# Optimization experiments

Measured on AMD Instinct MI355X. Metric: run time of the kernel, lower is better.

The kernel has to match this reference:

```python
import jax, jax.numpy as jnp
import numpy as np

B, H, IN = 2048, 256, 64
K_TERMS = 8


def setup_inputs() -> dict:
    key = jax.random.key(0)
    ks = jax.random.split(key, 8)
    limit_x = float(np.sqrt(6.0 / (IN + H)))
    limit_h = float(np.sqrt(6.0 / (H + H)))
    return {
        "h": jax.random.normal(ks[0], (B, H), dtype=jnp.float32),
        "x": jax.random.normal(ks[1], (B, IN), dtype=jnp.float32),
        "xdot": jax.random.normal(ks[2], (B, IN), dtype=jnp.float32),
        "wx": jax.random.uniform(ks[3], (H, IN), minval=-limit_x, maxval=limit_x, dtype=jnp.float32),
        "wh": jax.random.uniform(ks[4], (H, H), minval=-limit_h, maxval=limit_h, dtype=jnp.float32),
        "wout": jax.random.uniform(ks[5], (H, H), minval=-limit_h, maxval=limit_h, dtype=jnp.float32),
        "b0": jnp.zeros((H,), dtype=jnp.float32),
        "b1": jnp.zeros((H,), dtype=jnp.float32),
    }


def reference(h, x, xdot, wx, wh, wout, b0, b1):
    # Batched version of the per-sample vector field (original is vmapped by the solver).
    l1 = x @ wx.T + h @ wh.T + b0                 # [B,H]
    relu_val = jax.nn.relu(l1)
    lout = relu_val @ wout.T + b1                 # [B,H]
    tanh_val = jnp.tanh(lout)
    dtanh = 1.0 - tanh_val ** 2                   # [B,H]
    drelu = (l1 > 0).astype(jnp.float32)          # activation == 'relu' (hard gate)
    # d_outer[b,i,j] = dtanh[b,i] * wout[i,j] * drelu[b,j]
    d_outer = dtanh[:, :, None] * wout[None, :, :] * drelu[:, None, :]  # [B,H,H]
    Jx = jnp.einsum('bhj,ji->bhi', d_outer, wx)   # [B,H,IN]
    Jh = jnp.einsum('bhj,ji->bhi', d_outer, wh)   # [B,H,H]
    jx = jnp.einsum('bhi,bi->bh', Jx, xdot)       # [B,H]
    h_dot = jx
    curr_term = jx
    for _ in range(K_TERMS):
        curr_term = jnp.einsum('bij,bj->bi', Jh, curr_term)
        h_dot = h_dot + curr_term
    return h_dot
```

## Files before the change

kernel.cpp:

```cpp
#include <hip/hip_runtime.h>
#include <math.h>

#define B_  2048
#define H_  256
#define IN_ 64

typedef __attribute__((ext_vector_type(8))) short bf8_t;
typedef __attribute__((ext_vector_type(4))) short s4_t;
typedef __attribute__((ext_vector_type(4))) float f4_t;

#define MFMA_BF16(a, b, c) __builtin_amdgcn_mfma_f32_16x16x32_bf16((a), (b), (c), 0, 0, 0)

__device__ __forceinline__ short f2bf(float f) {
  union { float f; unsigned u; } v; v.f = f;
  unsigned u = v.u + 0x7fffu + ((v.u >> 16) & 1u);
  return (short)(u >> 16);
}
__device__ __forceinline__ float bf2f(short s) {
  union { unsigned u; float f; } v; v.u = ((unsigned)(unsigned short)s) << 16;
  return v.f;
}

__device__ __align__(16) short g_whf[2][65536];
__device__ __align__(16) short g_wof[2][65536];
__device__ __align__(16) short g_wxf[2][16384];

__global__ void prep_frag(const float* __restrict__ wh, const float* __restrict__ wo,
                          const float* __restrict__ wx) {
  int tid = blockIdx.x * 256 + threadIdx.x;
  const float* W; short* Dh; short* Dl; int ld, ksh, o8;
  if (tid < 8192)       { W = wh; Dh = g_whf[0]; Dl = g_whf[1]; ld = 256; ksh = 3; o8 = tid; }
  else if (tid < 16384) { W = wo; Dh = g_wof[0]; Dl = g_wof[1]; ld = 256; ksh = 3; o8 = tid - 8192; }
  else if (tid < 18432) { W = wx; Dh = g_wxf[0]; Dl = g_wxf[1]; ld = 64;  ksh = 1; o8 = tid - 16384; }
  else return;
  int lane = o8 & 63;
  int gks = o8 >> 6;
  int g = gks >> ksh, ks = gks & ((1 << ksh) - 1);
  int c = g * 16 + (lane & 15);
  int k0 = ks * 32 + ((lane >> 4) & 3) * 8;
  const float* p = W + (size_t)c * ld + k0;
  bf8_t hi, lo;
#pragma unroll
  for (int j = 0; j < 8; ++j) {
    float f = p[j];
    short h = f2bf(f);
    hi[j] = h; lo[j] = f2bf(f - bf2f(h));
  }
  *reinterpret_cast<bf8_t*>(Dh + (size_t)o8 * 8) = hi;
  *reinterpret_cast<bf8_t*>(Dl + (size_t)o8 * 8) = lo;
}

#define GEMM3(A0, A1, AH, AL, WH, WL, NK) do {                                  \
  f4_t q0 = {0.f,0.f,0.f,0.f}, q1 = {0.f,0.f,0.f,0.f};                          \
  _Pragma("unroll")                                                             \
  for (int ks = 0; ks < (NK); ++ks) {                                           \
    bf8_t ah = *reinterpret_cast<const bf8_t*>(&AH[ln][ks * 32 + lq * 8]);      \
    bf8_t al = *reinterpret_cast<const bf8_t*>(&AL[ln][ks * 32 + lq * 8]);      \
    if (ks & 1) {                                                               \
      q0 = MFMA_BF16(ah, WH[0][ks], q0); q0 = MFMA_BF16(ah, WL[0][ks], q0);     \
      q0 = MFMA_BF16(al, WH[0][ks], q0);                                        \
      q1 = MFMA_BF16(ah, WH[1][ks], q1); q1 = MFMA_BF16(ah, WL[1][ks], q1);     \
      q1 = MFMA_BF16(al, WH[1][ks], q1);                                        \
    } else {                                                                    \
      A0 = MFMA_BF16(ah, WH[0][ks], A0); A0 = MFMA_BF16(ah, WL[0][ks], A0);     \
      A0 = MFMA_BF16(al, WH[0][ks], A0);                                        \
      A1 = MFMA_BF16(ah, WH[1][ks], A1); A1 = MFMA_BF16(ah, WL[1][ks], A1);     \
      A1 = MFMA_BF16(al, WH[1][ks], A1);                                        \
    }                                                                           \
  }                                                                             \
  A0 = A0 + q0; A1 = A1 + q1; } while (0)

#define GEMM2(A0, A1, AH, AL, WH, NK) do {                                      \
  f4_t q0 = {0.f,0.f,0.f,0.f}, q1 = {0.f,0.f,0.f,0.f};                          \
  _Pragma("unroll")                                                             \
  for (int ks = 0; ks < (NK); ++ks) {                                           \
    bf8_t ah = *reinterpret_cast<const bf8_t*>(&AH[ln][ks * 32 + lq * 8]);      \
    bf8_t al = *reinterpret_cast<const bf8_t*>(&AL[ln][ks * 32 + lq * 8]);      \
    if (ks & 1) {                                                               \
      q0 = MFMA_BF16(ah, WH[0][ks], q0); q0 = MFMA_BF16(al, WH[0][ks], q0);     \
      q1 = MFMA_BF16(ah, WH[1][ks], q1); q1 = MFMA_BF16(al, WH[1][ks], q1);     \
    } else {                                                                    \
      A0 = MFMA_BF16(ah, WH[0][ks], A0); A0 = MFMA_BF16(al, WH[0][ks], A0);     \
      A1 = MFMA_BF16(ah, WH[1][ks], A1); A1 = MFMA_BF16(al, WH[1][ks], A1);     \
    }                                                                           \
  }                                                                             \
  A0 = A0 + q0; A1 = A1 + q1; } while (0)

#define GEMM1(A0, A1, AH, WH, NK) do {                                          \
  f4_t q0 = {0.f,0.f,0.f,0.f}, q1 = {0.f,0.f,0.f,0.f};                          \
  _Pragma("unroll")                                                             \
  for (int ks = 0; ks < (NK); ++ks) {                                           \
    bf8_t ah = *reinterpret_cast<const bf8_t*>(&AH[ln][ks * 32 + lq * 8]);      \
    if (ks & 1) {                                                               \
      q0 = MFMA_BF16(ah, WH[0][ks], q0);                                        \
      q1 = MFMA_BF16(ah, WH[1][ks], q1);                                        \
    } else {                                                                    \
      A0 = MFMA_BF16(ah, WH[0][ks], A0);                                        \
      A1 = MFMA_BF16(ah, WH[1][ks], A1);                                        \
    }                                                                           \
  }                                                                             \
  A0 = A0 + q0; A1 = A1 + q1; } while (0)

__global__ __launch_bounds__(512, 2) void jacde_mfma(
    const float* __restrict__ h_g, const float* __restrict__ x_g,
    const float* __restrict__ xd_g, const float* __restrict__ wx,
    const float* __restrict__ wh, const float* __restrict__ b0,
    const float* __restrict__ b1, float* __restrict__ out) {

  __shared__ short h_hi[16][264], h_lo[16][264];
  __shared__ short x_hi[16][72],  x_lo[16][72];
  __shared__ short xd_hi[16][72], xd_lo[16][72];
  __shared__ short u_hi[16][264], u_lo[16][264];
  __shared__ short v_hi[16][264];
  __shared__ float l1_t[16][264];
  __shared__ int   fix_cnt;
  __shared__ int   fix_list[64];

  const int tid  = threadIdx.x;
  const int wv   = tid >> 6;
  const int lane = tid & 63;
  const int ln   = lane & 15;
  const int lq   = lane >> 4;
  const int r0   = blockIdx.x * 16;
  const int cbase = wv * 32;

  if (tid == 0) fix_cnt = 0;

  for (int c = tid; c < 16 * 64; c += 512) {
    int r = c >> 6, k4 = (c & 63) * 4;
    f4_t v = *reinterpret_cast<const f4_t*>(h_g + (size_t)(r0 + r) * H_ + k4);
    s4_t shv, slv;
#pragma unroll
    for (int j = 0; j < 4; ++j) { short h = f2bf(v[j]); shv[j] = h; slv[j] = f2bf(v[j] - bf2f(h)); }
    *reinterpret_cast<s4_t*>(&h_hi[r][k4]) = shv;
    *reinterpret_cast<s4_t*>(&h_lo[r][k4]) = slv;
  }
  {
    int t2 = tid & 255;
    const float* src = (tid < 256) ? x_g : xd_g;
    short (*dh)[72] = (tid < 256) ? x_hi : xd_hi;
    short (*dl)[72] = (tid < 256) ? x_lo : xd_lo;
    int r = t2 >> 4, k4 = (t2 & 15) * 4;
    f4_t v = *reinterpret_cast<const f4_t*>(src + (size_t)(r0 + r) * IN_ + k4);
    s4_t shv, slv;
#pragma unroll
    for (int j = 0; j < 4; ++j) { short h = f2bf(v[j]); shv[j] = h; slv[j] = f2bf(v[j] - bf2f(h)); }
    *reinterpret_cast<s4_t*>(&dh[r][k4]) = shv;
    *reinterpret_cast<s4_t*>(&dl[r][k4]) = slv;
  }

  bf8_t whf[2][8], wof[2][8];
  f4_t acc0, acc1, sacc0, sacc1;
  float dre0[4], dre1[4], dta0[4], dta1[4], hd0[4], hd1[4];

  {
    bf8_t whl[2][8], wxh[2][2], wxl[2][2];
#pragma unroll
    for (int t = 0; t < 2; ++t) {
      int gb = wv * 2 + t;
#pragma unroll
      for (int ks = 0; ks < 8; ++ks) {
        int off = ((gb * 8 + ks) * 64 + lane) * 8;
        whf[t][ks] = *reinterpret_cast<const bf8_t*>(&g_whf[0][off]);
        whl[t][ks] = *reinterpret_cast<const bf8_t*>(&g_whf[1][off]);
      }
#pragma unroll
      for (int ks = 0; ks < 2; ++ks) {
        int off = ((gb * 2 + ks) * 64 + lane) * 8;
        wxh[t][ks] = *reinterpret_cast<const bf8_t*>(&g_wxf[0][off]);
        wxl[t][ks] = *reinterpret_cast<const bf8_t*>(&g_wxf[1][off]);
      }
    }
    __syncthreads();

    float bv0 = b0[cbase + ln], bv1 = b0[cbase + 16 + ln];
    acc0 = (f4_t){bv0, bv0, bv0, bv0};
    acc1 = (f4_t){bv1, bv1, bv1, bv1};
    GEMM3(acc0, acc1, h_hi, h_lo, whf, whl, 8);
    GEMM3(acc0, acc1, x_hi, x_lo, wxh, wxl, 2);
    sacc0 = (f4_t){0.f, 0.f, 0.f, 0.f};
    sacc1 = (f4_t){0.f, 0.f, 0.f, 0.f};
    GEMM3(sacc0, sacc1, xd_hi, xd_lo, wxh, wxl, 2);
#pragma unroll
    for (int r = 0; r < 4; ++r) {
      l1_t[lq * 4 + r][cbase + ln]      = acc0[r];
      l1_t[lq * 4 + r][cbase + 16 + ln] = acc1[r];
    }
  }
  __syncthreads();

  for (int e = tid; e < 16 * 256; e += 512) {
    int r = e >> 8, c = e & 255;
    if (fabsf(l1_t[r][c]) < 1e-4f) {
      int idx = atomicAdd(&fix_cnt, 1);
      if (idx < 64) fix_list[idx] = (r << 8) | c;
    }
  }
  __syncthreads();
  {
    int nfix = min(fix_cnt, 64);
    for (int e = wv; e < nfix; e += 8) {
      int rc = fix_list[e];
      int r = rc >> 8, c = rc & 255;
      const float* hrow = h_g + (size_t)(r0 + r) * H_;
      const float* wrow = wh + (size_t)c * H_;
      double sum = (double)hrow[lane]       * (double)wrow[lane]
                 + (double)hrow[lane + 64]  * (double)wrow[lane + 64]
                 + (double)hrow[lane + 128] * (double)wrow[lane + 128]
                 + (double)hrow[lane + 192] * (double)wrow[lane + 192]
                 + (double)x_g[(size_t)(r0 + r) * IN_ + lane] * (double)wx[(size_t)c * IN_ + lane];
#pragma unroll
      for (int m = 32; m; m >>= 1) sum += __shfl_xor(sum, m);
      if (lane == 0) l1_t[r][c] = (float)(sum + (double)b0[c]);
    }
  }
  __syncthreads();

  for (int e = tid; e < 16 * 256; e += 512) {
    int r = e >> 8, c = e & 255;
    float l1 = l1_t[r][c];
    float rv = l1 > 0.f ? l1 : 0.f;
    short hi = f2bf(rv);
    u_hi[r][c] = hi;
    u_lo[r][c] = f2bf(rv - bf2f(hi));
  }
#pragma unroll
  for (int r = 0; r < 4; ++r) {
    dre0[r] = (l1_t[lq * 4 + r][cbase + ln]      > 0.f) ? 1.f : 0.f;
    dre1[r] = (l1_t[lq * 4 + r][cbase + 16 + ln] > 0.f) ? 1.f : 0.f;
  }
  __syncthreads();

  {
    bf8_t wol[2][8];
#pragma unroll
    for (int t = 0; t < 2; ++t) {
      int gb = wv * 2 + t;
#pragma unroll
      for (int ks = 0; ks < 8; ++ks) {
        int off = ((gb * 8 + ks) * 64 + lane) * 8;
        wof[t][ks] = *reinterpret_cast<const bf8_t*>(&g_wof[0][off]);
        wol[t][ks] = *reinterpret_cast<const bf8_t*>(&g_wof[1][off]);
      }
    }
    float bv0 = b1[cbase + ln], bv1 = b1[cbase + 16 + ln];
    acc0 = (f4_t){bv0, bv0, bv0, bv0};
    acc1 = (f4_t){bv1, bv1, bv1, bv1};
    GEMM3(acc0, acc1, u_hi, u_lo, wof, wol, 8);
#pragma unroll
    for (int r = 0; r < 4; ++r) {
      float t0 = tanhf(acc0[r]);
      float t1 = tanhf(acc1[r]);
      dta0[r] = 1.f - t0 * t0;
      dta1[r] = 1.f - t1 * t1;
    }
  }
  __syncthreads();

#pragma unroll
  for (int r = 0; r < 4; ++r) {
    int row = lq * 4 + r;
    float v0 = dre0[r] * sacc0[r];
    float v1 = dre1[r] * sacc1[r];
    short h0 = f2bf(v0), h1 = f2bf(v1);
    u_hi[row][cbase + ln]      = h0;  u_lo[row][cbase + ln]      = f2bf(v0 - bf2f(h0));
    u_hi[row][cbase + 16 + ln] = h1;  u_lo[row][cbase + 16 + ln] = f2bf(v1 - bf2f(h1));
  }
  __syncthreads();

  acc0 = (f4_t){0.f, 0.f, 0.f, 0.f};
  acc1 = (f4_t){0.f, 0.f, 0.f, 0.f};
  GEMM2(acc0, acc1, u_hi, u_lo, wof, 8);
#pragma unroll
  for (int r = 0; r < 4; ++r) {
    int row = lq * 4 + r;
    float v0 = dta0[r] * acc0[r];
    float v1 = dta1[r] * acc1[r];
    hd0[r] = v0; hd1[r] = v1;
    v_hi[row][cbase + ln]      = f2bf(v0);
    v_hi[row][cbase + 16 + ln] = f2bf(v1);
  }
  __syncthreads();

  for (int it = 0; it < 8; ++it) {
    acc0 = (f4_t){0.f, 0.f, 0.f, 0.f};
    acc1 = (f4_t){0.f, 0.f, 0.f, 0.f};
    GEMM1(acc0, acc1, v_hi, whf, 8);
#pragma unroll
    for (int r = 0; r < 4; ++r) {
      int row = lq * 4 + r;
      u_hi[row][cbase + ln]      = f2bf(dre0[r] * acc0[r]);
      u_hi[row][cbase + 16 + ln] = f2bf(dre1[r] * acc1[r]);
    }
    __syncthreads();

    acc0 = (f4_t){0.f, 0.f, 0.f, 0.f};
    acc1 = (f4_t){0.f, 0.f, 0.f, 0.f};
    GEMM1(acc0, acc1, u_hi, wof, 8);
#pragma unroll
    for (int r = 0; r < 4; ++r) {
      int row = lq * 4 + r;
      float v0 = dta0[r] * acc0[r];
      float v1 = dta1[r] * acc1[r];
      hd0[r] += v0; hd1[r] += v1;
      if (it < 7) {
        v_hi[row][cbase + ln]      = f2bf(v0);
        v_hi[row][cbase + 16 + ln] = f2bf(v1);
      }
    }
    __syncthreads();
  }

#pragma unroll
  for (int r = 0; r < 4; ++r) {
    int row = lq * 4 + r;
    out[(size_t)(r0 + row) * H_ + cbase + ln]      = hd0[r];
    out[(size_t)(r0 + row) * H_ + cbase + 16 + ln] = hd1[r];
  }
}

extern "C" void kernel_launch(void* const* d_in, const int* in_sizes, int n_in,
                              void* d_out, int out_size, void* d_ws, size_t ws_size,
                              hipStream_t stream) {
  const float* h_g  = (const float*)d_in[0];
  const float* x_g  = (const float*)d_in[1];
  const float* xd_g = (const float*)d_in[2];
  const float* wx   = (const float*)d_in[3];
  const float* wh   = (const float*)d_in[4];
  const float* wo   = (const float*)d_in[5];
  const float* b0   = (const float*)d_in[6];
  const float* b1   = (const float*)d_in[7];
  prep_frag<<<dim3(72), dim3(256), 0, stream>>>(wh, wo, wx);
  jacde_mfma<<<dim3(B_ / 16), dim3(512), 0, stream>>>(
      h_g, x_g, xd_g, wx, wh, b0, b1, (float*)d_out);
}
```

Before: 89.51 us.

## Split each block's columns over 16 waves with one 16-column tile per wave

Doubles the block from 512 to 1024 threads so each of 16 wavefronts owns one 16-column MFMA tile instead of two. Register-resident weight fragments per wave are halved, and the serial iteration chain is spread across more waves per block to raise latency hiding. In exchange each wave issues half as many independent MFMA chains, and barriers now synchronise twice as many waves. Occupancy limits and register pressure also change with the new launch bounds.

Result: no change. 90.94 us (+1.6%).

```diff
diff --git a/kernel.cpp b/kernel.cpp
--- a/kernel.cpp
+++ b/kernel.cpp
@@ -50,58 +50,44 @@
   *reinterpret_cast<bf8_t*>(Dl + (size_t)o8 * 8) = lo;
 }
 
-#define GEMM3(A0, A1, AH, AL, WH, WL, NK) do {                                  \
-  f4_t q0 = {0.f,0.f,0.f,0.f}, q1 = {0.f,0.f,0.f,0.f};                          \
+#define GEMM3s(A0, AH, AL, WH, WL, NK) do {                                     \
+  f4_t q0 = {0.f,0.f,0.f,0.f};                                                  \
   _Pragma("unroll")                                                             \
   for (int ks = 0; ks < (NK); ++ks) {                                           \
     bf8_t ah = *reinterpret_cast<const bf8_t*>(&AH[ln][ks * 32 + lq * 8]);      \
     bf8_t al = *reinterpret_cast<const bf8_t*>(&AL[ln][ks * 32 + lq * 8]);      \
     if (ks & 1) {                                                               \
-      q0 = MFMA_BF16(ah, WH[0][ks], q0); q0 = MFMA_BF16(ah, WL[0][ks], q0);     \
-      q0 = MFMA_BF16(al, WH[0][ks], q0);                                        \
-      q1 = MFMA_BF16(ah, WH[1][ks], q1); q1 = MFMA_BF16(ah, WL[1][ks], q1);     \
-      q1 = MFMA_BF16(al, WH[1][ks], q1);                                        \
+      q0 = MFMA_BF16(ah, WH[ks], q0); q0 = MFMA_BF16(ah, WL[ks], q0);           \
+      q0 = MFMA_BF16(al, WH[ks], q0);                                           \
     } else {                                                                    \
-      A0 = MFMA_BF16(ah, WH[0][ks], A0); A0 = MFMA_BF16(ah, WL[0][ks], A0);     \
-      A0 = MFMA_BF16(al, WH[0][ks], A0);                                        \
-      A1 = MFMA_BF16(ah, WH[1][ks], A1); A1 = MFMA_BF16(ah, WL[1][ks], A1);     \
-      A1 = MFMA_BF16(al, WH[1][ks], A1);                                        \
+      A0 = MFMA_BF16(ah, WH[ks], A0); A0 = MFMA_BF16(ah, WL[ks], A0);           \
+      A0 = MFMA_BF16(al, WH[ks], A0);                                           \
     }                                                                           \
   }                                                                             \
-  A0 = A0 + q0; A1 = A1 + q1; } while (0)
-
-#define GEMM2(A0, A1, AH, AL, WH, NK) do {                                      \
-  f4_t q0 = {0.f,0.f,0.f,0.f}, q1 = {0.f,0.f,0.f,0.f};                          \
+  A0 = A0 + q0; } while (0)
+
+#define GEMM2s(A0, AH, AL, WH, NK) do {                                         \
+  f4_t q0 = {0.f,0.f,0.f,0.f};                                                  \
   _Pragma("unroll")                                                             \
   for (int ks = 0; ks < (NK); ++ks) {                                           \
     bf8_t ah = *reinterpret_cast<const bf8_t*>(&AH[ln][ks * 32 + lq * 8]);      \
     bf8_t al = *reinterpret_cast<const bf8_t*>(&AL[ln][ks * 32 + lq * 8]);      \
-    if (ks & 1) {                                                               \
-      q0 = MFMA_BF16(ah, WH[0][ks], q0); q0 = MFMA_BF16(al, WH[0][ks], q0);     \
-      q1 = MFMA_BF16(ah, WH[1][ks], q1); q1 = MFMA_BF16(al, WH[1][ks], q1);     \
-    } else {                                                                    \
-      A0 = MFMA_BF16(ah, WH[0][ks], A0); A0 = MFMA_BF16(al, WH[0][ks], A0);     \
-      A1 = MFMA_BF16(ah, WH[1][ks], A1); A1 = MFMA_BF16(al, WH[1][ks], A1);     \
-    }                                                                           \
+    if (ks & 1) { q0 = MFMA_BF16(ah, WH[ks], q0); q0 = MFMA_BF16(al, WH[ks], q0); } \
+    else        { A0 = MFMA_BF16(ah, WH[ks], A0); A0 = MFMA_BF16(al, WH[ks], A0); } \
   }                                                                             \
-  A0 = A0 + q0; A1 = A1 + q1; } while (0)
-
-#define GEMM1(A0, A1, AH, WH, NK) do {                                          \
-  f4_t q0 = {0.f,0.f,0.f,0.f}, q1 = {0.f,0.f,0.f,0.f};                          \
+  A0 = A0 + q0; } while (0)
+
+#define GEMM1s(A0, AH, WH, NK) do {                                             \
+  f4_t q0 = {0.f,0.f,0.f,0.f};                                                  \
   _Pragma("unroll")                                                             \
   for (int ks = 0; ks < (NK); ++ks) {                                           \
     bf8_t ah = *reinterpret_cast<const bf8_t*>(&AH[ln][ks * 32 + lq * 8]);      \
-    if (ks & 1) {                                                               \
-      q0 = MFMA_BF16(ah, WH[0][ks], q0);                                        \
-      q1 = MFMA_BF16(ah, WH[1][ks], q1);                                        \
-    } else {                                                                    \
-      A0 = MFMA_BF16(ah, WH[0][ks], A0);                                        \
-      A1 = MFMA_BF16(ah, WH[1][ks], A1);                                        \
-    }                                                                           \
+    if (ks & 1) q0 = MFMA_BF16(ah, WH[ks], q0);                                 \
+    else        A0 = MFMA_BF16(ah, WH[ks], A0);                                 \
   }                                                                             \
-  A0 = A0 + q0; A1 = A1 + q1; } while (0)
-
-__global__ __launch_bounds__(512, 2) void jacde_mfma(
+  A0 = A0 + q0; } while (0)
+
+__global__ __launch_bounds__(1024, 4) void jacde_mfma(
     const float* __restrict__ h_g, const float* __restrict__ x_g,
     const float* __restrict__ xd_g, const float* __restrict__ wx,
     const float* __restrict__ wh, const float* __restrict__ b0,
@@ -122,12 +108,12 @@
   const int ln   = lane & 15;
   const int lq   = lane >> 4;
   const int r0   = blockIdx.x * 16;
-  const int cbase = wv * 32;
+  const int cbase = wv * 16;
 
   if (tid == 0) fix_cnt = 0;
 
-  for (int c = tid; c < 16 * 64; c += 512) {
-    int r = c >> 6, k4 = (c & 63) * 4;
+  {
+    int r = tid >> 6, k4 = (tid & 63) * 4;
     f4_t v = *reinterpret_cast<const f4_t*>(h_g + (size_t)(r0 + r) * H_ + k4);
     s4_t shv, slv;
 #pragma unroll
@@ -135,7 +121,7 @@
     *reinterpret_cast<s4_t*>(&h_hi[r][k4]) = shv;
     *reinterpret_cast<s4_t*>(&h_lo[r][k4]) = slv;
   }
-  {
+  if (tid < 512) {
     int t2 = tid & 255;
     const float* src = (tid < 256) ? x_g : xd_g;
     short (*dh)[72] = (tid < 256) ? x_hi : xd_hi;
@@ -149,47 +135,39 @@
     *reinterpret_cast<s4_t*>(&dl[r][k4]) = slv;
   }
 
-  bf8_t whf[2][8], wof[2][8];
-  f4_t acc0, acc1, sacc0, sacc1;
-  float dre0[4], dre1[4], dta0[4], dta1[4], hd0[4], hd1[4];
-
-  {
-    bf8_t whl[2][8], wxh[2][2], wxl[2][2];
-#pragma unroll
-    for (int t = 0; t < 2; ++t) {
-      int gb = wv * 2 + t;
-#pragma unroll
-      for (int ks = 0; ks < 8; ++ks) {
-        int off = ((gb * 8 + ks) * 64 + lane) * 8;
-        whf[t][ks] = *reinterpret_cast<const bf8_t*>(&g_whf[0][off]);
-        whl[t][ks] = *reinterpret_cast<const bf8_t*>(&g_whf[1][off]);
-      }
-#pragma unroll
-      for (int ks = 0; ks < 2; ++ks) {
-        int off = ((gb * 2 + ks) * 64 + lane) * 8;
-        wxh[t][ks] = *reinterpret_cast<const bf8_t*>(&g_wxf[0][off]);
-        wxl[t][ks] = *reinterpret_cast<const bf8_t*>(&g_wxf[1][off]);
-      }
+  bf8_t whf[8], wof[8];
+  f4_t acc0, sacc0;
+  float dre0[4], dta0[4], hd0[4];
+
+  {
+    bf8_t whl[8], wxh[2], wxl[2];
+#pragma unroll
+    for (int ks = 0; ks < 8; ++ks) {
+      int off = ((wv * 8 + ks) * 64 + lane) * 8;
+      whf[ks] = *reinterpret_cast<const bf8_t*>(&g_whf[0][off]);
+      whl[ks] = *reinterpret_cast<const bf8_t*>(&g_whf[1][off]);
+    }
+#pragma unroll
+    for (int ks = 0; ks < 2; ++ks) {
+      int off = ((wv * 2 + ks) * 64 + lane) * 8;
+      wxh[ks] = *reinterpret_cast<const bf8_t*>(&g_wxf[0][off]);
+      wxl[ks] = *reinterpret_cast<const bf8_t*>(&g_wxf[1][off]);
     }
     __syncthreads();
 
-    float bv0 = b0[cbase + ln], bv1 = b0[cbase + 16 + ln];
+    float bv0 = b0[cbase + ln];
     acc0 = (f4_t){bv0, bv0, bv0, bv0};
-    acc1 = (f4_t){bv1, bv1, bv1, bv1};
-    GEMM3(acc0, acc1, h_hi, h_lo, whf, whl, 8);
-    GEMM3(acc0, acc1, x_hi, x_lo, wxh, wxl, 2);
+    GEMM3s(acc0, h_hi, h_lo, whf, whl, 8);
+    GEMM3s(acc0, x_hi, x_lo, wxh, wxl, 2);
     sacc0 = (f4_t){0.f, 0.f, 0.f, 0.f};
-    sacc1 = (f4_t){0.f, 0.f, 0.f, 0.f};
-    GEMM3(sacc0, sacc1, xd_hi, xd_lo, wxh, wxl, 2);
-#pragma unroll
-    for (int r = 0; r < 4; ++r) {
-      l1_t[lq * 4 + r][cbase + ln]      = acc0[r];
-      l1_t[lq * 4 + r][cbase + 16 + ln] = acc1[r];
-    }
-  }
-  __syncthreads();
-
-  for (int e = tid; e < 16 * 256; e += 512) {
+    GEMM3s(sacc0, xd_hi, xd_lo, wxh, wxl, 2);
+#pragma unroll
+    for (int r = 0; r < 4; ++r)
+      l1_t[lq * 4 + r][cbase + ln] = acc0[r];
+  }
+  __syncthreads();
+
+  for (int e = tid; e < 16 * 256; e += 1024) {
     int r = e >> 8, c = e & 255;
     if (fabsf(l1_t[r][c]) < 1e-4f) {
       int idx = atomicAdd(&fix_cnt, 1);
@@ -199,7 +177,7 @@
   __syncthreads();
   {
     int nfix = min(fix_cnt, 64);
-    for (int e = wv; e < nfix; e += 8) {
+    for (int e = wv; e < nfix; e += 16) {
       int rc = fix_list[e];
       int r = rc >> 8, c = rc & 255;
       const float* hrow = h_g + (size_t)(r0 + r) * H_;
@@ -216,7 +194,7 @@
   }
   __syncthreads();
 
-  for (int e = tid; e < 16 * 256; e += 512) {
+  for (int e = tid; e < 16 * 256; e += 1024) {
     int r = e >> 8, c = e & 255;
     float l1 = l1_t[r][c];
     float rv = l1 > 0.f ? l1 : 0.f;
@@ -225,34 +203,25 @@
     u_lo[r][c] = f2bf(rv - bf2f(hi));
   }
 #pragma unroll
-  for (int r = 0; r < 4; ++r) {
-    dre0[r] = (l1_t[lq * 4 + r][cbase + ln]      > 0.f) ? 1.f : 0.f;
-    dre1[r] = (l1_t[lq * 4 + r][cbase + 16 + ln] > 0.f) ? 1.f : 0.f;
-  }
-  __syncthreads();
-
-  {
-    bf8_t wol[2][8];
-#pragma unroll
-    for (int t = 0; t < 2; ++t) {
-      int gb = wv * 2 + t;
-#pragma unroll
-      for (int ks = 0; ks < 8; ++ks) {
-        int off = ((gb * 8 + ks) * 64 + lane) * 8;
-        wof[t][ks] = *reinterpret_cast<const bf8_t*>(&g_wof[0][off]);
-        wol[t][ks] = *reinterpret_cast<const bf8_t*>(&g_wof[1][off]);
-      }
-    }
-    float bv0 = b1[cbase + ln], bv1 = b1[cbase + 16 + ln];
+  for (int r = 0; r < 4; ++r)
+    dre0[r] = (l1_t[lq * 4 + r][cbase + ln] > 0.f) ? 1.f : 0.f;
+  __syncthreads();
+
+  {
+    bf8_t wol[8];
+#pragma unroll
+    for (int ks = 0; ks < 8; ++ks) {
+      int off = ((wv * 8 + ks) * 64 + lane) * 8;
+      wof[ks] = *reinterpret_cast<const bf8_t*>(&g_wof[0][off]);
+      wol[ks] = *reinterpret_cast<const bf8_t*>(&g_wof[1][off]);
+    }
+    float bv0 = b1[cbase + ln];
     acc0 = (f4_t){bv0, bv0, bv0, bv0};
-    acc1 = (f4_t){bv1, bv1, bv1, bv1};
-    GEMM3(acc0, acc1, u_hi, u_lo, wof, wol, 8);
+    GEMM3s(acc0, u_hi, u_lo, wof, wol, 8);
 #pragma unroll
     for (int r = 0; r < 4; ++r) {
       float t0 = tanhf(acc0[r]);
-      float t1 = tanhf(acc1[r]);
       dta0[r] = 1.f - t0 * t0;
-      dta1[r] = 1.f - t1 * t1;
     }
   }
   __syncthreads();
@@ -261,62 +230,45 @@
   for (int r = 0; r < 4; ++r) {
     int row = lq * 4 + r;
     float v0 = dre0[r] * sacc0[r];
-    float v1 = dre1[r] * sacc1[r];
-    short h0 = f2bf(v0), h1 = f2bf(v1);
-    u_hi[row][cbase + ln]      = h0;  u_lo[row][cbase + ln]      = f2bf(v0 - bf2f(h0));
-    u_hi[row][cbase + 16 + ln] = h1;  u_lo[row][cbase + 16 + ln] = f2bf(v1 - bf2f(h1));
+    short h0 = f2bf(v0);
+    u_hi[row][cbase + ln] = h0;
+    u_lo[row][cbase + ln] = f2bf(v0 - bf2f(h0));
   }
   __syncthreads();
 
   acc0 = (f4_t){0.f, 0.f, 0.f, 0.f};
-  acc1 = (f4_t){0.f, 0.f, 0.f, 0.f};
-  GEMM2(acc0, acc1, u_hi, u_lo, wof, 8);
+  GEMM2s(acc0, u_hi, u_lo, wof, 8);
 #pragma unroll
   for (int r = 0; r < 4; ++r) {
     int row = lq * 4 + r;
     float v0 = dta0[r] * acc0[r];
-    float v1 = dta1[r] * acc1[r];
-    hd0[r] = v0; hd1[r] = v1;
-    v_hi[row][cbase + ln]      = f2bf(v0);
-    v_hi[row][cbase + 16 + ln] = f2bf(v1);
+    hd0[r] = v0;
+    v_hi[row][cbase + ln] = f2bf(v0);
   }
   __syncthreads();
 
   for (int it = 0; it < 8; ++it) {
     acc0 = (f4_t){0.f, 0.f, 0.f, 0.f};
-    acc1 = (f4_t){0.f, 0.f, 0.f, 0.f};
-    GEMM1(acc0, acc1, v_hi, whf, 8);
+    GEMM1s(acc0, v_hi, whf, 8);
+#pragma unroll
+    for (int r = 0; r < 4; ++r)
+      u_hi[lq * 4 + r][cbase + ln] = f2bf(dre0[r] * acc0[r]);
+    __syncthreads();
+
+    acc0 = (f4_t){0.f, 0.f, 0.f, 0.f};
+    GEMM1s(acc0, u_hi, wof, 8);
 #pragma unroll
     for (int r = 0; r < 4; ++r) {
-      int row = lq * 4 + r;
-      u_hi[row][cbase + ln]      = f2bf(dre0[r] * acc0[r]);
-      u_hi[row][cbase + 16 + ln] = f2bf(dre1[r] * acc1[r]);
+      float v0 = dta0[r] * acc0[r];
+      hd0[r] += v0;
+      if (it < 7) v_hi[lq * 4 + r][cbase + ln] = f2bf(v0);
     }
     __syncthreads();
-
-    acc0 = (f4_t){0.f, 0.f, 0.f, 0.f};
-    acc1 = (f4_t){0.f, 0.f, 0.f, 0.f};
-    GEMM1(acc0, acc1, u_hi, wof, 8);
-#pragma unroll
-    for (int r = 0; r < 4; ++r) {
-      int row = lq * 4 + r;
-      float v0 = dta0[r] * acc0[r];
-      float v1 = dta1[r] * acc1[r];
-      hd0[r] += v0; hd1[r] += v1;
-      if (it < 7) {
-        v_hi[row][cbase + ln]      = f2bf(v0);
-        v_hi[row][cbase + 16 + ln] = f2bf(v1);
-      }
-    }
-    __syncthreads();
-  }
-
-#pragma unroll
-  for (int r = 0; r < 4; ++r) {
-    int row = lq * 4 + r;
-    out[(size_t)(r0 + row) * H_ + cbase + ln]      = hd0[r];
-    out[(size_t)(r0 + row) * H_ + cbase + 16 + ln] = hd1[r];
-  }
+  }
+
+#pragma unroll
+  for (int r = 0; r < 4; ++r)
+    out[(size_t)(r0 + lq * 4 + r) * H_ + cbase + ln] = hd0[r];
 }
 
 extern "C" void kernel_launch(void* const* d_in, const int* in_sizes, int n_in,
@@ -331,6 +283,6 @@
   const float* b0   = (const float*)d_in[6];
   const float* b1   = (const float*)d_in[7];
   prep_frag<<<dim3(72), dim3(256), 0, stream>>>(wh, wo, wx);
-  jacde_mfma<<<dim3(B_ / 16), dim3(512), 0, stream>>>(
+  jacde_mfma<<<dim3(B_ / 16), dim3(1024), 0, stream>>>(
       h_g, x_g, xd_g, wx, wh, b0, b1, (float*)d_out);
 }
```

## Fuse weight-fragment prep into main kernel with grid-wide atomic barrier

Applied to the files above, without the earlier changes.

Removes the separate prep_frag launch. Each of the 128 blocks converts a slice of the weight matrices into bf16 hi/lo fragments, then waits on a global atomic counter until all blocks have finished before loading the fragments. The counter resets itself at kernel end. Near-zero detection of l1 is also folded into the GEMM epilogue, which drops a shared-memory scan and a barrier. This saves one launch gap, but it relies on all 128 blocks being co-resident (the barrier deadlocks otherwise) and adds a spin-wait.

New measurement: 106.6 us. 19.0% more time.

```diff
diff --git a/kernel.cpp b/kernel.cpp
--- a/kernel.cpp
+++ b/kernel.cpp
@@ -24,31 +24,7 @@
 __device__ __align__(16) short g_whf[2][65536];
 __device__ __align__(16) short g_wof[2][65536];
 __device__ __align__(16) short g_wxf[2][16384];
-
-__global__ void prep_frag(const float* __restrict__ wh, const float* __restrict__ wo,
-                          const float* __restrict__ wx) {
-  int tid = blockIdx.x * 256 + threadIdx.x;
-  const float* W; short* Dh; short* Dl; int ld, ksh, o8;
-  if (tid < 8192)       { W = wh; Dh = g_whf[0]; Dl = g_whf[1]; ld = 256; ksh = 3; o8 = tid; }
-  else if (tid < 16384) { W = wo; Dh = g_wof[0]; Dl = g_wof[1]; ld = 256; ksh = 3; o8 = tid - 8192; }
-  else if (tid < 18432) { W = wx; Dh = g_wxf[0]; Dl = g_wxf[1]; ld = 64;  ksh = 1; o8 = tid - 16384; }
-  else return;
-  int lane = o8 & 63;
-  int gks = o8 >> 6;
-  int g = gks >> ksh, ks = gks & ((1 << ksh) - 1);
-  int c = g * 16 + (lane & 15);
-  int k0 = ks * 32 + ((lane >> 4) & 3) * 8;
-  const float* p = W + (size_t)c * ld + k0;
-  bf8_t hi, lo;
-#pragma unroll
-  for (int j = 0; j < 8; ++j) {
-    float f = p[j];
-    short h = f2bf(f);
-    hi[j] = h; lo[j] = f2bf(f - bf2f(h));
-  }
-  *reinterpret_cast<bf8_t*>(Dh + (size_t)o8 * 8) = hi;
-  *reinterpret_cast<bf8_t*>(Dl + (size_t)o8 * 8) = lo;
-}
+__device__ int g_cnt;
 
 #define GEMM3(A0, A1, AH, AL, WH, WL, NK) do {                                  \
   f4_t q0 = {0.f,0.f,0.f,0.f}, q1 = {0.f,0.f,0.f,0.f};                          \
@@ -104,8 +80,9 @@
 __global__ __launch_bounds__(512, 2) void jacde_mfma(
     const float* __restrict__ h_g, const float* __restrict__ x_g,
     const float* __restrict__ xd_g, const float* __restrict__ wx,
-    const float* __restrict__ wh, const float* __restrict__ b0,
-    const float* __restrict__ b1, float* __restrict__ out) {
+    const float* __restrict__ wh, const float* __restrict__ wo,
+    const float* __restrict__ b0, const float* __restrict__ b1,
+    float* __restrict__ out) {
 
   __shared__ short h_hi[16][264], h_lo[16][264];
   __shared__ short x_hi[16][72],  x_lo[16][72];
@@ -149,6 +126,38 @@
     *reinterpret_cast<s4_t*>(&dl[r][k4]) = slv;
   }
 
+  if (tid < 144) {
+    int gid = blockIdx.x * 144 + tid;
+    const float* W; short* Dh; short* Dl; int ld, ksh, o8;
+    if (gid < 8192)       { W = wh; Dh = g_whf[0]; Dl = g_whf[1]; ld = 256; ksh = 3; o8 = gid; }
+    else if (gid < 16384) { W = wo; Dh = g_wof[0]; Dl = g_wof[1]; ld = 256; ksh = 3; o8 = gid - 8192; }
+    else                  { W = wx; Dh = g_wxf[0]; Dl = g_wxf[1]; ld = 64;  ksh = 1; o8 = gid - 16384; }
+    int l2 = o8 & 63;
+    int gks = o8 >> 6;
+    int g = gks >> ksh, ks = gks & ((1 << ksh) - 1);
+    int c = g * 16 + (l2 & 15);
+    int k0 = ks * 32 + ((l2 >> 4) & 3) * 8;
+    const float* p = W + (size_t)c * ld + k0;
+    bf8_t hi, lo;
+#pragma unroll
+    for (int j = 0; j < 8; ++j) {
+      float f = p[j];
+      short h = f2bf(f);
+      hi[j] = h; lo[j] = f2bf(f - bf2f(h));
+    }
+    *reinterpret_cast<bf8_t*>(Dh + (size_t)o8 * 8) = hi;
+    *reinterpret_cast<bf8_t*>(Dl + (size_t)o8 * 8) = lo;
+    __threadfence();
+  }
+  __syncthreads();
+
+  if (tid == 0) {
+    __hip_atomic_fetch_add(&g_cnt, 1, __ATOMIC_RELEASE, __HIP_MEMORY_SCOPE_AGENT);
+    while (__hip_atomic_load(&g_cnt, __ATOMIC_ACQUIRE, __HIP_MEMORY_SCOPE_AGENT) < 128)
+      __builtin_amdgcn_s_sleep(2);
+  }
+  __syncthreads();
+
   bf8_t whf[2][8], wof[2][8];
   f4_t acc0, acc1, sacc0, sacc1;
   float dre0[4], dre1[4], dta0[4], dta1[4], hd0[4], hd1[4];
@@ -171,7 +180,6 @@
         wxl[t][ks] = *reinterpret_cast<const bf8_t*>(&g_wxf[1][off]);
       }
     }
-    __syncthreads();
 
     float bv0 = b0[cbase + ln], bv1 = b0[cbase + 16 + ln];
     acc0 = (f4_t){bv0, bv0, bv0, bv0};
@@ -185,18 +193,18 @@
     for (int r = 0; r < 4; ++r) {
       l1_t[lq * 4 + r][cbase + ln]      = acc0[r];
       l1_t[lq * 4 + r][cbase + 16 + ln] = acc1[r];
-    }
-  }
-  __syncthreads();
-
-  for (int e = tid; e < 16 * 256; e += 512) {
-    int r = e >> 8, c = e & 255;
-    if (fabsf(l1_t[r][c]) < 1e-4f) {
-      int idx = atomicAdd(&fix_cnt, 1);
-      if (idx < 64) fix_list[idx] = (r << 8) | c;
-    }
-  }
-  __syncthreads();
+      if (fabsf(acc0[r]) < 1e-4f) {
+        int idx = atomicAdd(&fix_cnt, 1);
+        if (idx < 64) fix_list[idx] = ((lq * 4 + r) << 8) | (cbase + ln);
+      }
+      if (fabsf(acc1[r]) < 1e-4f) {
+        int idx = atomicAdd(&fix_cnt, 1);
+        if (idx < 64) fix_list[idx] = ((lq * 4 + r) << 8) | (cbase + 16 + ln);
+      }
+    }
+  }
+  __syncthreads();
+
   {
     int nfix = min(fix_cnt, 64);
     for (int e = wv; e < nfix; e += 8) {
@@ -317,6 +325,12 @@
     out[(size_t)(r0 + row) * H_ + cbase + ln]      = hd0[r];
     out[(size_t)(r0 + row) * H_ + cbase + 16 + ln] = hd1[r];
   }
+
+  if (tid == 0) {
+    int old = __hip_atomic_fetch_add(&g_cnt, 1, __ATOMIC_RELAXED, __HIP_MEMORY_SCOPE_AGENT);
+    if (old == 255)
+      __hip_atomic_store(&g_cnt, 0, __ATOMIC_RELAXED, __HIP_MEMORY_SCOPE_AGENT);
+  }
 }
 
 extern "C" void kernel_launch(void* const* d_in, const int* in_sizes, int n_in,
@@ -330,7 +344,6 @@
   const float* wo   = (const float*)d_in[5];
   const float* b0   = (const float*)d_in[6];
   const float* b1   = (const float*)d_in[7];
-  prep_frag<<<dim3(72), dim3(256), 0, stream>>>(wh, wo, wx);
   jacde_mfma<<<dim3(B_ / 16), dim3(512), 0, stream>>>(
-      h_g, x_g, xd_g, wx, wh, b0, b1, (float*)d_out);
+      h_g, x_g, xd_g, wx, wh, wo, b0, b1, (float*)d_out);
 }
```

## Fuse fix-detection, relu staging and second GEMM to remove block barriers

Applied to the files above, without the earlier changes.

Near-zero l1 detection moves into the GEMM epilogue using register values, so the separate scan pass and its barrier go away. The Wout fragment loads are hoisted ahead of the first barrier. The relu input and the gated xdot projection are staged together in one pass, reusing the h buffers, and the first Jacobian-vector GEMM is fused with the tanh GEMM. Its output goes into the l1_t region aliased as bf16, which drops several __syncthreads and shared-memory passes. In exchange it holds more registers live (wol across the fix phase) and relies on shared-memory aliasing.

Result: no change. 89.35 us (-0.2%).

```diff
diff --git a/kernel.cpp b/kernel.cpp
--- a/kernel.cpp
+++ b/kernel.cpp
@@ -116,6 +116,8 @@
   __shared__ int   fix_cnt;
   __shared__ int   fix_list[64];
 
+  short (*vb)[264] = reinterpret_cast<short (*)[264]>(l1_t);
+
   const int tid  = threadIdx.x;
   const int wv   = tid >> 6;
   const int lane = tid & 63;
@@ -149,7 +151,7 @@
     *reinterpret_cast<s4_t*>(&dl[r][k4]) = slv;
   }
 
-  bf8_t whf[2][8], wof[2][8];
+  bf8_t whf[2][8], wof[2][8], wol[2][8];
   f4_t acc0, acc1, sacc0, sacc1;
   float dre0[4], dre1[4], dta0[4], dta1[4], hd0[4], hd1[4];
 
@@ -185,18 +187,29 @@
     for (int r = 0; r < 4; ++r) {
       l1_t[lq * 4 + r][cbase + ln]      = acc0[r];
       l1_t[lq * 4 + r][cbase + 16 + ln] = acc1[r];
+      if (fabsf(acc0[r]) < 1e-4f) {
+        int idx = atomicAdd(&fix_cnt, 1);
+        if (idx < 64) fix_list[idx] = ((lq * 4 + r) << 8) | (cbase + ln);
+      }
+      if (fabsf(acc1[r]) < 1e-4f) {
+        int idx = atomicAdd(&fix_cnt, 1);
+        if (idx < 64) fix_list[idx] = ((lq * 4 + r) << 8) | (cbase + 16 + ln);
+      }
+    }
+  }
+
+#pragma unroll
+  for (int t = 0; t < 2; ++t) {
+    int gb = wv * 2 + t;
+#pragma unroll
+    for (int ks = 0; ks < 8; ++ks) {
+      int off = ((gb * 8 + ks) * 64 + lane) * 8;
+      wof[t][ks] = *reinterpret_cast<const bf8_t*>(&g_wof[0][off]);
+      wol[t][ks] = *reinterpret_cast<const bf8_t*>(&g_wof[1][off]);
     }
   }
   __syncthreads();
 
-  for (int e = tid; e < 16 * 256; e += 512) {
-    int r = e >> 8, c = e & 255;
-    if (fabsf(l1_t[r][c]) < 1e-4f) {
-      int idx = atomicAdd(&fix_cnt, 1);
-      if (idx < 64) fix_list[idx] = (r << 8) | c;
-    }
-  }
-  __syncthreads();
   {
     int nfix = min(fix_cnt, 64);
     for (int e = wv; e < nfix; e += 8) {
@@ -216,76 +229,55 @@
   }
   __syncthreads();
 
-  for (int e = tid; e < 16 * 256; e += 512) {
-    int r = e >> 8, c = e & 255;
-    float l1 = l1_t[r][c];
-    float rv = l1 > 0.f ? l1 : 0.f;
-    short hi = f2bf(rv);
-    u_hi[r][c] = hi;
-    u_lo[r][c] = f2bf(rv - bf2f(hi));
-  }
 #pragma unroll
   for (int r = 0; r < 4; ++r) {
-    dre0[r] = (l1_t[lq * 4 + r][cbase + ln]      > 0.f) ? 1.f : 0.f;
-    dre1[r] = (l1_t[lq * 4 + r][cbase + 16 + ln] > 0.f) ? 1.f : 0.f;
+    int row = lq * 4 + r;
+    float l10 = l1_t[row][cbase + ln];
+    float l11 = l1_t[row][cbase + 16 + ln];
+    dre0[r] = (l10 > 0.f) ? 1.f : 0.f;
+    dre1[r] = (l11 > 0.f) ? 1.f : 0.f;
+    float rv0 = l10 > 0.f ? l10 : 0.f;
+    float rv1 = l11 > 0.f ? l11 : 0.f;
+    short rh0 = f2bf(rv0), rh1 = f2bf(rv1);
+    u_hi[row][cbase + ln]      = rh0;  u_lo[row][cbase + ln]      = f2bf(rv0 - bf2f(rh0));
+    u_hi[row][cbase + 16 + ln] = rh1;  u_lo[row][cbase + 16 + ln] = f2bf(rv1 - bf2f(rh1));
+    float u00 = dre0[r] * sacc0[r];
+    float u01 = dre1[r] * sacc1[r];
+    short uh0 = f2bf(u00), uh1 = f2bf(u01);
+    h_hi[row][cbase + ln]      = uh0;  h_lo[row][cbase + ln]      = f2bf(u00 - bf2f(uh0));
+    h_hi[row][cbase + 16 + ln] = uh1;  h_lo[row][cbase + 16 + ln] = f2bf(u01 - bf2f(uh1));
   }
   __syncthreads();
 
   {
-    bf8_t wol[2][8];
-#pragma unroll
-    for (int t = 0; t < 2; ++t) {
-      int gb = wv * 2 + t;
-#pragma unroll
-      for (int ks = 0; ks < 8; ++ks) {
-        int off = ((gb * 8 + ks) * 64 + lane) * 8;
-        wof[t][ks] = *reinterpret_cast<const bf8_t*>(&g_wof[0][off]);
-        wol[t][ks] = *reinterpret_cast<const bf8_t*>(&g_wof[1][off]);
-      }
-    }
     float bv0 = b1[cbase + ln], bv1 = b1[cbase + 16 + ln];
     acc0 = (f4_t){bv0, bv0, bv0, bv0};
     acc1 = (f4_t){bv1, bv1, bv1, bv1};
     GEMM3(acc0, acc1, u_hi, u_lo, wof, wol, 8);
+    sacc0 = (f4_t){0.f, 0.f, 0.f, 0.f};
+    sacc1 = (f4_t){0.f, 0.f, 0.f, 0.f};
+    GEMM2(sacc0, sacc1, h_hi, h_lo, wof, 8);
 #pragma unroll
     for (int r = 0; r < 4; ++r) {
       float t0 = tanhf(acc0[r]);
       float t1 = tanhf(acc1[r]);
       dta0[r] = 1.f - t0 * t0;
       dta1[r] = 1.f - t1 * t1;
+      int row = lq * 4 + r;
+      float v0 = dta0[r] * sacc0[r];
+      float v1 = dta1[r] * sacc1[r];
+      hd0[r] = v0; hd1[r] = v1;
+      vb[row][cbase + ln]      = f2bf(v0);
+      vb[row][cbase + 16 + ln] = f2bf(v1);
     }
   }
   __syncthreads();
 
-#pragma unroll
-  for (int r = 0; r < 4; ++r) {
-    int row = lq * 4 + r;
-    float v0 = dre0[r] * sacc0[r];
-    float v1 = dre1[r] * sacc1[r];
-    short h0 = f2bf(v0), h1 = f2bf(v1);
-    u_hi[row][cbase + ln]      = h0;  u_lo[row][cbase + ln]      = f2bf(v0 - bf2f(h0));
-    u_hi[row][cbase + 16 + ln] = h1;  u_lo[row][cbase + 16 + ln] = f2bf(v1 - bf2f(h1));
-  }
-  __syncthreads();
-
-  acc0 = (f4_t){0.f, 0.f, 0.f, 0.f};
-  acc1 = (f4_t){0.f, 0.f, 0.f, 0.f};
-  GEMM2(acc0, acc1, u_hi, u_lo, wof, 8);
-#pragma unroll
-  for (int r = 0; r < 4; ++r) {
-    int row = lq * 4 + r;
-    float v0 = dta0[r] * acc0[r];
-    float v1 = dta1[r] * acc1[r];
-    hd0[r] = v0; hd1[r] = v1;
-    v_hi[row][cbase + ln]      = f2bf(v0);
-    v_hi[row][cbase + 16 + ln] = f2bf(v1);
-  }
-  __syncthreads();
-
+  const short (*vsrc)[264] = vb;
   for (int it = 0; it < 8; ++it) {
     acc0 = (f4_t){0.f, 0.f, 0.f, 0.f};
     acc1 = (f4_t){0.f, 0.f, 0.f, 0.f};
-    GEMM1(acc0, acc1, v_hi, whf, 8);
+    GEMM1(acc0, acc1, vsrc, whf, 8);
 #pragma unroll
     for (int r = 0; r < 4; ++r) {
       int row = lq * 4 + r;
@@ -308,6 +300,7 @@
         v_hi[row][cbase + 16 + ln] = f2bf(v1);
       }
     }
+    vsrc = v_hi;
     __syncthreads();
   }
 
```
